# Performance work log

Measured on AMD Instinct MI355X. Metric: run time of the kernel, lower is better.

## Reference

```python
import jax, jax.numpy as jnp
import numpy as np

SPATIAL_SHAPES = [(128, 128), (64, 64), (32, 32), (16, 16)]  # (H_l, W_l) per level
NUM_HEADS = 8
NUM_LEVELS = 4
NUM_POINTS = 4
EMBED_DIM = 256
HEAD_DIM = EMBED_DIM // NUM_HEADS
LEN_V = sum(h * w for h, w in SPATIAL_SHAPES)  # 21760
BS, LQ = 8, 900


def setup_inputs() -> dict:
    key = jax.random.key(0)
    ks = jax.random.split(key, 12)
    s = 0.05
    return {
        'query': jax.random.normal(ks[0], (BS, LQ, EMBED_DIM), jnp.float32),
        'reference_points': jax.random.uniform(ks[1], (BS, LQ, NUM_LEVELS, 2), jnp.float32),
        'value': jax.random.normal(ks[2], (BS, LEN_V, EMBED_DIM), jnp.float32),
        'w_value': jax.random.normal(ks[3], (EMBED_DIM, EMBED_DIM), jnp.float32) * s,
        'b_value': jnp.zeros((EMBED_DIM,), jnp.float32),
        'w_off': jax.random.normal(ks[4], (EMBED_DIM, NUM_HEADS * NUM_LEVELS * NUM_POINTS * 2), jnp.float32) * s,
        'b_off': jax.random.normal(ks[5], (NUM_HEADS * NUM_LEVELS * NUM_POINTS * 2,), jnp.float32),
        'w_attn': jax.random.normal(ks[6], (EMBED_DIM, NUM_HEADS * NUM_LEVELS * NUM_POINTS), jnp.float32) * s,
        'b_attn': jnp.zeros((NUM_HEADS * NUM_LEVELS * NUM_POINTS,), jnp.float32),
        'w_out': jax.random.normal(ks[7], (EMBED_DIM, EMBED_DIM), jnp.float32) * s,
        'b_out': jnp.zeros((EMBED_DIM,), jnp.float32),
    }


def _bilinear_sample(val, locx, locy, H, W):
    # val: [bs, nh, H*W, hd]; locx/locy: [bs, nh, N] normalized in [0,1]
    # grid_sample semantics: align_corners=False, zero padding.
    px = locx * W - 0.5
    py = locy * H - 0.5
    x0 = jnp.floor(px)
    y0 = jnp.floor(py)
    dx = px - x0
    dy = py - y0
    x0i = x0.astype(jnp.int32)
    y0i = y0.astype(jnp.int32)
    out = jnp.zeros(val.shape[:2] + (locx.shape[-1], val.shape[-1]), val.dtype)
    corners = [
        (x0i, y0i, (1 - dx) * (1 - dy)),
        (x0i + 1, y0i, dx * (1 - dy)),
        (x0i, y0i + 1, (1 - dx) * dy),
        (x0i + 1, y0i + 1, dx * dy),
    ]
    for xi, yi, w in corners:
        valid = ((xi >= 0) & (xi < W) & (yi >= 0) & (yi < H)).astype(val.dtype)
        idx = jnp.clip(yi, 0, H - 1) * W + jnp.clip(xi, 0, W - 1)
        g = jnp.take_along_axis(val, idx[..., None], axis=2)  # [bs,nh,N,hd]
        out = out + g * (w * valid)[..., None]
    return out


def reference(query, reference_points, value, w_value, b_value, w_off, b_off,
              w_attn, b_attn, w_out, b_out):
    bs, Lq, C = query.shape
    # value projection -> [bs, Lv, nh, hd]
    v = (value @ w_value + b_value).reshape(bs, -1, NUM_HEADS, HEAD_DIM)
    # sampling offsets [bs,Lq,nh,L,P,2], attention weights softmax over L*P
    off = (query @ w_off + b_off).reshape(bs, Lq, NUM_HEADS, NUM_LEVELS, NUM_POINTS, 2)
    aw = (query @ w_attn + b_attn).reshape(bs, Lq, NUM_HEADS, NUM_LEVELS * NUM_POINTS)
    aw = jax.nn.softmax(aw, axis=-1).reshape(bs, Lq, NUM_HEADS, NUM_LEVELS, NUM_POINTS)
    # normalizer is (W_l, H_l) per level (flip of spatial shapes)
    norm = jnp.asarray([[w, h] for h, w in SPATIAL_SHAPES], query.dtype)  # [L,2]
    loc = reference_points[:, :, None, :, None, :] + off / norm[None, None, None, :, None, :]
    # per-level bilinear sampling and weighted reduction
    out = jnp.zeros((bs, Lq, NUM_HEADS, HEAD_DIM), query.dtype)
    start = 0
    for l, (H, W) in enumerate(SPATIAL_SHAPES):
        vl = v[:, start:start + H * W]                       # [bs,HW,nh,hd]
        vl = vl.transpose(0, 2, 1, 3)                        # [bs,nh,HW,hd]
        ll = loc[:, :, :, l].transpose(0, 2, 1, 3, 4)        # [bs,nh,Lq,P,2]
        ll = ll.reshape(bs, NUM_HEADS, Lq * NUM_POINTS, 2)
        s = _bilinear_sample(vl, ll[..., 0], ll[..., 1], H, W)
        s = s.reshape(bs, NUM_HEADS, Lq, NUM_POINTS, HEAD_DIM)
        out = out + jnp.einsum('bhqpd,bqhp->bqhd', s, aw[:, :, :, l])
        start += H * W
    out = out.reshape(bs, Lq, C)
    return out @ w_out + b_out
```

## Files before the change

### kernel.cpp

```cpp
#include <hip/hip_runtime.h>

#define BS 8
#define LQ 900
#define NH 8
#define NL 4
#define NP 4
#define HD 32
#define ED 256
#define LEN_V 21760

#define QB 32
#define QCHUNKS 29

typedef __attribute__((ext_vector_type(8))) short bf16x8;
typedef __attribute__((ext_vector_type(4))) float f32x4;
typedef __attribute__((ext_vector_type(4))) float fv4;

static __device__ __forceinline__ unsigned short f2bf(float f) {
  union { float f; unsigned u; } x; x.f = f;
  unsigned r = x.u + 0x7fffu + ((x.u >> 16) & 1u);
  return (unsigned short)(r >> 16);
}
static __device__ __forceinline__ float bf_lo(unsigned u) {
  union { unsigned u; float f; } x; x.u = u << 16;
  return x.f;
}
static __device__ __forceinline__ float bf_hi(unsigned u) {
  union { unsigned u; float f; } x; x.u = u & 0xffff0000u;
  return x.f;
}
static __device__ __forceinline__ unsigned pack2(float a, float b) {
  return (unsigned)f2bf(a) | ((unsigned)f2bf(b) << 16);
}

__global__ __launch_bounds__(256) void bprep_kernel(
    const float* __restrict__ w, unsigned short* __restrict__ Bsw) {
  const int id = blockIdx.x * 256 + threadIdx.x;
  const int n = id & 255;
  const int kseg = (id >> 8) & 3;
  const int kc = id >> 10;
  const float* src = &w[(kc * 32 + kseg * 8) * 256 + n];
  float f[8];
#pragma unroll
  for (int j = 0; j < 8; j++) f[j] = src[j * 256];
  uint4 pk;
  pk.x = pack2(f[0], f[1]);
  pk.y = pack2(f[2], f[3]);
  pk.z = pack2(f[4], f[5]);
  pk.w = pack2(f[6], f[7]);
  *(uint4*)&Bsw[((kc * 4 + kseg) * 256 + n) * 8] = pk;
}

__global__ __launch_bounds__(256, 4) void vproj_kernel(
    const float* __restrict__ value, const unsigned short* __restrict__ Bsw,
    const float* __restrict__ bias, unsigned short* __restrict__ vout) {
  const int t = threadIdx.x;
  const int row0 = blockIdx.x * 64;
  const int wv = t >> 6;
  const int lane = t & 63;
  const int quad = lane >> 4;
  const int nn = lane & 15;

  __shared__ unsigned short a_lds[4 * 64 * 8];

  f32x4 acc[4][4];
#pragma unroll
  for (int i = 0; i < 4; i++)
#pragma unroll
    for (int j = 0; j < 4; j++) acc[i][j] = (f32x4)(0.f);

  const int arow = t >> 2;
  const int akseg = t & 3;
  const unsigned short* bptr = &Bsw[(quad * 256 + wv * 64 + nn) * 8];

  for (int kc = 0; kc < 8; kc++) {
    __syncthreads();
    {
      const float* pa = &value[(row0 + arow) * 256 + kc * 32 + akseg * 8];
      fv4 v0 = __builtin_nontemporal_load((const fv4*)pa);
      fv4 v1 = __builtin_nontemporal_load((const fv4*)(pa + 4));
      uint4 pk;
      pk.x = pack2(v0.x, v0.y);
      pk.y = pack2(v0.z, v0.w);
      pk.z = pack2(v1.x, v1.y);
      pk.w = pack2(v1.z, v1.w);
      *(uint4*)&a_lds[(akseg * 64 + arow) * 8] = pk;
    }
    __syncthreads();

    bf16x8 af[4], bfr[4];
#pragma unroll
    for (int ct = 0; ct < 4; ct++)
      bfr[ct] = *(const bf16x8*)(bptr + (kc * 1024 + ct * 16) * 8);
#pragma unroll
    for (int rt = 0; rt < 4; rt++)
      af[rt] = *(const bf16x8*)&a_lds[(quad * 64 + rt * 16 + nn) * 8];
#pragma unroll
    for (int rt = 0; rt < 4; rt++)
#pragma unroll
      for (int ct = 0; ct < 4; ct++)
        acc[rt][ct] = __builtin_amdgcn_mfma_f32_16x16x32_bf16(
            af[rt], bfr[ct], acc[rt][ct], 0, 0, 0);
  }

  const int bb = row0 / LEN_V;
  const int s0 = row0 - bb * LEN_V;
#pragma unroll
  for (int ct = 0; ct < 4; ct++) {
    const int col = wv * 64 + ct * 16 + nn;
    const float bv = bias[col];
    const int h = col >> 5;
    const int d = col & 31;
    unsigned short* vb = &vout[((bb * NH + h) * LEN_V + s0) * HD + d];
#pragma unroll
    for (int rt = 0; rt < 4; rt++) {
      f32x4 f = acc[rt][ct];
#pragma unroll
      for (int reg = 0; reg < 4; reg++) {
        const int s = rt * 16 + quad * 4 + reg;
        vb[s * HD] = f2bf(f[reg] + bv);
      }
    }
  }
}

__global__ __launch_bounds__(256, 4) void samp_kernel(
    const float* __restrict__ query, const float* __restrict__ refp,
    const unsigned short* __restrict__ vp,
    const float* __restrict__ w_off, const float* __restrict__ b_off,
    const float* __restrict__ w_attn, const float* __restrict__ b_attn,
    float* __restrict__ RES) {
  const int t = threadIdx.x;
  const int work = (blockIdx.x & 7) * (8 * QCHUNKS) + (blockIdx.x >> 3);
  const int pair = work / QCHUNKS;
  const int qc   = work - pair * QCHUNKS;
  const int b = pair >> 3;
  const int h = pair & 7;
  const int q0 = qc * QB;

  __shared__ __align__(16) unsigned char smem[39936];
  float* q_ldsf = (float*)smem;
  int   (*soff)[4] = (int(*)[4])smem;
  float (*swt)[4]  = (float(*)[4])(smem + 8192);
  float (*off_lds)[32] = (float(*)[32])(smem + 32768);
  float (*aw_lds)[16]  = (float(*)[16])(smem + 32768 + 4096);
  float (*ref_lds)[4][2] = (float(*)[4][2])(smem + 32768 + 6144);

#pragma unroll
  for (int k = 0; k < 8; k++) {
    const int f = t + k * 256;
    const int row = f >> 6;
    const int c4i = (f & 63) << 2;
    float4 v = (q0 + row < LQ)
        ? *(const float4*)&query[(b * LQ + q0 + row) * 256 + c4i]
        : make_float4(0.f, 0.f, 0.f, 0.f);
    *(float4*)&q_ldsf[row * 256 + c4i] = v;
  }
  {
    const int q = t >> 3, l = (t >> 1) & 3, xy = t & 1;
    ref_lds[q][l][xy] = (q0 + q < LQ)
        ? refp[((b * LQ + q0 + q) * NL + l) * 2 + xy] : 0.5f;
  }
  __syncthreads();

  if (t < 192) {
    const int rg = t / 12;
    const int c4 = t % 12;
    const int col = c4 * 4;
    const bool isOff = col < 32;
    const float* wbase = isOff ? (w_off + h * 32 + col)
                               : (w_attn + h * 16 + (col - 32));
    const int wstride = isOff ? 256 : 128;
    const float* bb = isOff ? (b_off + h * 32 + col)
                            : (b_attn + h * 16 + (col - 32));

    float4 acc[2];
    acc[0] = make_float4(0.f, 0.f, 0.f, 0.f);
    acc[1] = make_float4(0.f, 0.f, 0.f, 0.f);

    for (int k0 = 0; k0 < 256; k0 += 8) {
      float4 wr[8];
#pragma unroll
      for (int k = 0; k < 8; k++)
        wr[k] = *(const float4*)&wbase[(k0 + k) * wstride];
#pragma unroll
      for (int r = 0; r < 2; r++) {
        const float* ar = &q_ldsf[(rg * 2 + r) * 256 + k0];
        float4 a0 = *(const float4*)&ar[0];
        float4 a1 = *(const float4*)&ar[4];
        float4 s = acc[r];
        s.x += a0.x*wr[0].x + a0.y*wr[1].x + a0.z*wr[2].x + a0.w*wr[3].x
             + a1.x*wr[4].x + a1.y*wr[5].x + a1.z*wr[6].x + a1.w*wr[7].x;
        s.y += a0.x*wr[0].y + a0.y*wr[1].y + a0.z*wr[2].y + a0.w*wr[3].y
             + a1.x*wr[4].y + a1.y*wr[5].y + a1.z*wr[6].y + a1.w*wr[7].y;
        s.z += a0.x*wr[0].z + a0.y*wr[1].z + a0.z*wr[2].z + a0.w*wr[3].z
             + a1.x*wr[4].z + a1.y*wr[5].z + a1.z*wr[6].z + a1.w*wr[7].z;
        s.w += a0.x*wr[0].w + a0.y*wr[1].w + a0.z*wr[2].w + a0.w*wr[3].w
             + a1.x*wr[4].w + a1.y*wr[5].w + a1.z*wr[6].w + a1.w*wr[7].w;
        acc[r] = s;
      }
    }

    const float4 bv = *(const float4*)bb;
#pragma unroll
    for (int r = 0; r < 2; r++) {
      const int q = rg * 2 + r;
      float4 o = make_float4(acc[r].x + bv.x, acc[r].y + bv.y,
                             acc[r].z + bv.z, acc[r].w + bv.w);
      if (isOff) *(float4*)&off_lds[q][col] = o;
      else       *(float4*)&aw_lds[q][col - 32] = o;
    }
  }
  __syncthreads();

  if (t < QB) {
    float* a = &aw_lds[t][0];
    float m = a[0];
#pragma unroll
    for (int i = 1; i < 16; i++) m = fmaxf(m, a[i]);
    float e[16];
    float ssum = 0.f;
#pragma unroll
    for (int i = 0; i < 16; i++) { e[i] = __expf(a[i] - m); ssum += e[i]; }
    const float inv = 1.f / ssum;
#pragma unroll
    for (int i = 0; i < 16; i++) a[i] = e[i] * inv;
  }
  __syncthreads();

#pragma unroll
  for (int ss = 0; ss < 2; ss++) {
    const int sid = t + ss * 256;
    const int p = sid & 3, l = (sid >> 2) & 3, q = sid >> 4;
    const int W = 128 >> l;
    const int base = (l == 0) ? 0 : ((l == 1) ? 16384 : ((l == 2) ? 20480 : 21504));
    const float Wf = (float)W;
    const float refx = ref_lds[q][l][0];
    const float refy = ref_lds[q][l][1];
    const float offx = off_lds[q][l * 8 + p * 2 + 0];
    const float offy = off_lds[q][l * 8 + p * 2 + 1];
    const float aw = aw_lds[q][l * 4 + p];
    const float px = refx * Wf + offx - 0.5f;
    const float py = refy * Wf + offy - 0.5f;
    const float x0f = floorf(px), y0f = floorf(py);
    const float dx = px - x0f, dy = py - y0f;
    const int x0 = (int)x0f, y0 = (int)y0f;
    const int x1 = x0 + 1, y1 = y0 + 1;
    const float mx0 = (x0 >= 0 && x0 < W) ? 1.f : 0.f;
    const float mx1 = (x1 >= 0 && x1 < W) ? 1.f : 0.f;
    const float my0 = (y0 >= 0 && y0 < W) ? 1.f : 0.f;
    const float my1 = (y1 >= 0 && y1 < W) ? 1.f : 0.f;
    const int x0c = min(max(x0, 0), W - 1);
    const int x1c = min(max(x1, 0), W - 1);
    const int y0c = min(max(y0, 0), W - 1);
    const int y1c = min(max(y1, 0), W - 1);
    soff[sid][0] = (base + y0c * W + x0c) * 8;
    soff[sid][1] = (base + y0c * W + x1c) * 8;
    soff[sid][2] = (base + y1c * W + x0c) * 8;
    soff[sid][3] = (base + y1c * W + x1c) * 8;
    swt[sid][0] = (1.f - dx) * (1.f - dy) * mx0 * my0 * aw;
    swt[sid][1] = dx * (1.f - dy) * mx1 * my0 * aw;
    swt[sid][2] = (1.f - dx) * dy * mx0 * my1 * aw;
    swt[sid][3] = dx * dy * mx1 * my1 * aw;
  }
  __syncthreads();

  const int q = t >> 3;
  const int d4 = t & 7;
  const uint2* vpu2 = (const uint2*)vp + (size_t)(b * NH + h) * (LEN_V * HD / 4);
  float r0 = 0.f, r1 = 0.f, r2 = 0.f, r3 = 0.f;
  const int sbase = q << 4;
#pragma unroll 4
  for (int lp = 0; lp < 16; lp++) {
    const int sid = sbase + lp;
    const int4 o = *(const int4*)&soff[sid][0];
    const float4 w = *(const float4*)&swt[sid][0];
    const uint2 u00 = vpu2[o.x + d4];
    const uint2 u10 = vpu2[o.y + d4];
    const uint2 u01 = vpu2[o.z + d4];
    const uint2 u11 = vpu2[o.w + d4];
    r0 += w.x * bf_lo(u00.x) + w.y * bf_lo(u10.x) + w.z * bf_lo(u01.x) + w.w * bf_lo(u11.x);
    r1 += w.x * bf_hi(u00.x) + w.y * bf_hi(u10.x) + w.z * bf_hi(u01.x) + w.w * bf_hi(u11.x);
    r2 += w.x * bf_lo(u00.y) + w.y * bf_lo(u10.y) + w.z * bf_lo(u01.y) + w.w * bf_lo(u11.y);
    r3 += w.x * bf_hi(u00.y) + w.y * bf_hi(u10.y) + w.z * bf_hi(u01.y) + w.w * bf_hi(u11.y);
  }
  if (q0 + q < LQ) {
    float4 rr = make_float4(r0, r1, r2, r3);
    *(float4*)&RES[(b * LQ + q0 + q) * 256 + h * 32 + d4 * 4] = rr;
  }
}

__global__ __launch_bounds__(256, 2) void outproj_kernel(
    const float* __restrict__ RES, const float* __restrict__ w,
    const float* __restrict__ bias, float* __restrict__ out) {
  const int t = threadIdx.x;
  const int row0 = blockIdx.x * 32;
  const int rg = t >> 6;
  const int c0 = (t & 63) << 2;
  __shared__ float a_lds[32][8];

  float4 acc[8];
#pragma unroll
  for (int r = 0; r < 8; r++) acc[r] = make_float4(0.f, 0.f, 0.f, 0.f);

  const int lr = t >> 3;
  const int lk = t & 7;
  for (int k0 = 0; k0 < 256; k0 += 8) {
    __syncthreads();
    a_lds[lr][lk] = RES[(row0 + lr) * 256 + k0 + lk];
    __syncthreads();
    float4 wr[8];
#pragma unroll
    for (int k = 0; k < 8; k++)
      wr[k] = *(const float4*)&w[(k0 + k) * 256 + c0];
#pragma unroll
    for (int r = 0; r < 8; r++) {
      const float* ar = &a_lds[rg * 8 + r][0];
      float4 a0 = *(const float4*)&ar[0];
      float4 a1 = *(const float4*)&ar[4];
      float4 s = acc[r];
      s.x += a0.x*wr[0].x + a0.y*wr[1].x + a0.z*wr[2].x + a0.w*wr[3].x
           + a1.x*wr[4].x + a1.y*wr[5].x + a1.z*wr[6].x + a1.w*wr[7].x;
      s.y += a0.x*wr[0].y + a0.y*wr[1].y + a0.z*wr[2].y + a0.w*wr[3].y
           + a1.x*wr[4].y + a1.y*wr[5].y + a1.z*wr[6].y + a1.w*wr[7].y;
      s.z += a0.x*wr[0].z + a0.y*wr[1].z + a0.z*wr[2].z + a0.w*wr[3].z
           + a1.x*wr[4].z + a1.y*wr[5].z + a1.z*wr[6].z + a1.w*wr[7].z;
      s.w += a0.x*wr[0].w + a0.y*wr[1].w + a0.z*wr[2].w + a0.w*wr[3].w
           + a1.x*wr[4].w + a1.y*wr[5].w + a1.z*wr[6].w + a1.w*wr[7].w;
      acc[r] = s;
    }
  }

  const float4 bv = *(const float4*)&bias[c0];
#pragma unroll
  for (int r = 0; r < 8; r++) {
    const int grow = row0 + rg * 8 + r;
    float4 o = make_float4(acc[r].x + bv.x, acc[r].y + bv.y,
                           acc[r].z + bv.z, acc[r].w + bv.w);
    *(float4*)&out[grow * 256 + c0] = o;
  }
}

extern "C" void kernel_launch(void* const* d_in, const int* in_sizes, int n_in,
                              void* d_out, int out_size, void* d_ws, size_t ws_size,
                              hipStream_t stream) {
  (void)in_sizes; (void)n_in; (void)out_size; (void)ws_size;
  const float* query   = (const float*)d_in[0];
  const float* refp    = (const float*)d_in[1];
  const float* value   = (const float*)d_in[2];
  const float* w_value = (const float*)d_in[3];
  const float* b_value = (const float*)d_in[4];
  const float* w_off   = (const float*)d_in[5];
  const float* b_off   = (const float*)d_in[6];
  const float* w_attn  = (const float*)d_in[7];
  const float* b_attn  = (const float*)d_in[8];
  const float* w_out   = (const float*)d_in[9];
  const float* b_out   = (const float*)d_in[10];
  float* out = (float*)d_out;

  char* ws = (char*)d_ws;
  unsigned short* vp  = (unsigned short*)ws;
  float* RES          = (float*)(ws + 89128960);
  unsigned short* Bsw = (unsigned short*)(ws + 89128960 + 7372800);

  bprep_kernel<<<32, 256, 0, stream>>>(w_value, Bsw);
  vproj_kernel<<<(BS * LEN_V) / 64, 256, 0, stream>>>(value, Bsw, b_value, vp);
  samp_kernel<<<64 * QCHUNKS, 256, 0, stream>>>(query, refp, vp,
                                                w_off, b_off, w_attn, b_attn,
                                                RES);
  outproj_kernel<<<(BS * LQ) / 32, 256, 0, stream>>>(RES, w_out, b_out, out);
}
```

Baseline: 412.0 us.

## Use 16-byte value gathers and split sampling points across thread pairs

The gather loop now has each thread load a uint4 (8 bf16 channels) per corner instead of a uint2. The 16 sampling points are split between two neighbouring threads, which combine their partial sums with a shuffle. The offset and weight tables in shared memory are transposed to [lp][q] so the per-point loads are laid out better across the wave. The aim is fewer, wider global load instructions and more memory-level parallelism per thread, at the cost of more registers and an extra cross-lane reduction.

```diff
diff --git a/kernel.cpp b/kernel.cpp
--- a/kernel.cpp
+++ b/kernel.cpp
@@ -140,8 +140,8 @@
 
   __shared__ __align__(16) unsigned char smem[39936];
   float* q_ldsf = (float*)smem;
-  int   (*soff)[4] = (int(*)[4])smem;
-  float (*swt)[4]  = (float(*)[4])(smem + 8192);
+  int   (*soffT)[32][4] = (int(*)[32][4])smem;
+  float (*swtT)[32][4]  = (float(*)[32][4])(smem + 8192);
   float (*off_lds)[32] = (float(*)[32])(smem + 32768);
   float (*aw_lds)[16]  = (float(*)[16])(smem + 32768 + 4096);
   float (*ref_lds)[4][2] = (float(*)[4][2])(smem + 32768 + 6144);
@@ -232,6 +232,7 @@
   for (int ss = 0; ss < 2; ss++) {
     const int sid = t + ss * 256;
     const int p = sid & 3, l = (sid >> 2) & 3, q = sid >> 4;
+    const int lp = sid & 15;
     const int W = 128 >> l;
     const int base = (l == 0) ? 0 : ((l == 1) ? 16384 : ((l == 2) ? 20480 : 21504));
     const float Wf = (float)W;
@@ -254,39 +255,52 @@
     const int x1c = min(max(x1, 0), W - 1);
     const int y0c = min(max(y0, 0), W - 1);
     const int y1c = min(max(y1, 0), W - 1);
-    soff[sid][0] = (base + y0c * W + x0c) * 8;
-    soff[sid][1] = (base + y0c * W + x1c) * 8;
-    soff[sid][2] = (base + y1c * W + x0c) * 8;
-    soff[sid][3] = (base + y1c * W + x1c) * 8;
-    swt[sid][0] = (1.f - dx) * (1.f - dy) * mx0 * my0 * aw;
-    swt[sid][1] = dx * (1.f - dy) * mx1 * my0 * aw;
-    swt[sid][2] = (1.f - dx) * dy * mx0 * my1 * aw;
-    swt[sid][3] = dx * dy * mx1 * my1 * aw;
+    soffT[lp][q][0] = (base + y0c * W + x0c) * 4;
+    soffT[lp][q][1] = (base + y0c * W + x1c) * 4;
+    soffT[lp][q][2] = (base + y1c * W + x0c) * 4;
+    soffT[lp][q][3] = (base + y1c * W + x1c) * 4;
+    swtT[lp][q][0] = (1.f - dx) * (1.f - dy) * mx0 * my0 * aw;
+    swtT[lp][q][1] = dx * (1.f - dy) * mx1 * my0 * aw;
+    swtT[lp][q][2] = (1.f - dx) * dy * mx0 * my1 * aw;
+    swtT[lp][q][3] = dx * dy * mx1 * my1 * aw;
   }
   __syncthreads();
 
-  const int q = t >> 3;
-  const int d4 = t & 7;
-  const uint2* vpu2 = (const uint2*)vp + (size_t)(b * NH + h) * (LEN_V * HD / 4);
-  float r0 = 0.f, r1 = 0.f, r2 = 0.f, r3 = 0.f;
-  const int sbase = q << 4;
-#pragma unroll 4
-  for (int lp = 0; lp < 16; lp++) {
-    const int sid = sbase + lp;
-    const int4 o = *(const int4*)&soff[sid][0];
-    const float4 w = *(const float4*)&swt[sid][0];
-    const uint2 u00 = vpu2[o.x + d4];
-    const uint2 u10 = vpu2[o.y + d4];
-    const uint2 u01 = vpu2[o.z + d4];
-    const uint2 u11 = vpu2[o.w + d4];
-    r0 += w.x * bf_lo(u00.x) + w.y * bf_lo(u10.x) + w.z * bf_lo(u01.x) + w.w * bf_lo(u11.x);
-    r1 += w.x * bf_hi(u00.x) + w.y * bf_hi(u10.x) + w.z * bf_hi(u01.x) + w.w * bf_hi(u11.x);
-    r2 += w.x * bf_lo(u00.y) + w.y * bf_lo(u10.y) + w.z * bf_lo(u01.y) + w.w * bf_lo(u11.y);
-    r3 += w.x * bf_hi(u00.y) + w.y * bf_hi(u10.y) + w.z * bf_hi(u01.y) + w.w * bf_hi(u11.y);
-  }
-  if (q0 + q < LQ) {
-    float4 rr = make_float4(r0, r1, r2, r3);
-    *(float4*)&RES[(b * LQ + q0 + q) * 256 + h * 32 + d4 * 4] = rr;
+  {
+    const int q = t >> 3;
+    const int d8 = (t >> 1) & 3;
+    const int lh = t & 1;
+    const uint4* vpu4 = (const uint4*)vp + (size_t)(b * NH + h) * (LEN_V * HD / 8);
+    float r[8];
+#pragma unroll
+    for (int j = 0; j < 8; j++) r[j] = 0.f;
+    const int lp0 = lh * 8;
+#pragma unroll
+    for (int i = 0; i < 8; i++) {
+      const int lp = lp0 + i;
+      const int4 o = *(const int4*)&soffT[lp][q][0];
+      const float4 w = *(const float4*)&swtT[lp][q][0];
+      const uint4 u00 = vpu4[o.x + d8];
+      const uint4 u10 = vpu4[o.y + d8];
+      const uint4 u01 = vpu4[o.z + d8];
+      const uint4 u11 = vpu4[o.w + d8];
+      r[0] += w.x * bf_lo(u00.x) + w.y * bf_lo(u10.x) + w.z * bf_lo(u01.x) + w.w * bf_lo(u11.x);
+      r[1] += w.x * bf_hi(u00.x) + w.y * bf_hi(u10.x) + w.z * bf_hi(u01.x) + w.w * bf_hi(u11.x);
+      r[2] += w.x * bf_lo(u00.y) + w.y * bf_lo(u10.y) + w.z * bf_lo(u01.y) + w.w * bf_lo(u11.y);
+      r[3] += w.x * bf_hi(u00.y) + w.y * bf_hi(u10.y) + w.z * bf_hi(u01.y) + w.w * bf_hi(u11.y);
+      r[4] += w.x * bf_lo(u00.z) + w.y * bf_lo(u10.z) + w.z * bf_lo(u01.z) + w.w * bf_lo(u11.z);
+      r[5] += w.x * bf_hi(u00.z) + w.y * bf_hi(u10.z) + w.z * bf_hi(u01.z) + w.w * bf_hi(u11.z);
+      r[6] += w.x * bf_lo(u00.w) + w.y * bf_lo(u10.w) + w.z * bf_lo(u01.w) + w.w * bf_lo(u11.w);
+      r[7] += w.x * bf_hi(u00.w) + w.y * bf_hi(u10.w) + w.z * bf_hi(u01.w) + w.w * bf_hi(u11.w);
+    }
+#pragma unroll
+    for (int j = 0; j < 8; j++) r[j] += __shfl_xor(r[j], 1);
+    if (q0 + q < LQ) {
+      const int dbase = d8 * 8 + lh * 4;
+      float4 rr = make_float4(r[lh * 4 + 0], r[lh * 4 + 1],
+                              r[lh * 4 + 2], r[lh * 4 + 3]);
+      *(float4*)&RES[(b * LQ + q0 + q) * 256 + h * 32 + dbase] = rr;
+    }
   }
 }
 
```

New measurement: 463.5 us. 12.5% more time.
